# Performance work log

Measured on AMD Instinct MI355X. Metric: run time of the kernel, lower is better.

The kernel has to match this reference:

```python
import jax, jax.numpy as jnp
import numpy as np

B, T, D = 2, 4096, 768
H = 12
DK = D // H


def setup_inputs() -> dict:
    key = jax.random.key(0)
    k1, k2, k3 = jax.random.split(key, 3)
    x = jax.random.normal(k1, (B, T, D), dtype=jnp.float32)
    W_qkv = jax.random.normal(k2, (D, 3 * D), dtype=jnp.float32) * (1.0 / np.sqrt(D))
    b_qkv = jnp.zeros((3 * D,), dtype=jnp.float32)
    W_proj = jax.random.normal(k3, (D, D), dtype=jnp.float32) * (1.0 / np.sqrt(D))
    b_proj = jnp.zeros((D,), dtype=jnp.float32)
    return {"x": x, "W_qkv": W_qkv, "b_qkv": b_qkv, "W_proj": W_proj, "b_proj": b_proj}


def reference(x, W_qkv, b_qkv, W_proj, b_proj):
    b, t, c = x.shape
    qkv = x @ W_qkv + b_qkv                      # [B,T,3D]
    q, k, v = jnp.split(qkv, 3, axis=-1)
    q = q.reshape(b, t, H, DK)                   # [B,T,H,DK]
    k = k.reshape(b, t, H, DK)
    v = v.reshape(b, t, H, DK)
    scale = 1.0 / np.sqrt(DK)
    scores = jnp.einsum('bthd,bshd->bhts', q, k) * scale   # [B,H,T,T]
    causal = jnp.tril(jnp.ones((t, t), dtype=bool))
    scores = jnp.where(causal[None, None], scores, jnp.float32(-jnp.inf))
    probs = jax.nn.softmax(scores, axis=-1)      # dropout p=0.0 -> identity
    out = jnp.einsum('bhts,bshd->bthd', probs, v).reshape(b, t, c)
    return out @ W_proj + b_proj
```

## Files before the change

kernel.cpp:

```cpp
#include <hip/hip_runtime.h>
#include <hip/hip_bf16.h>
#include <cstdint>
#include <cstddef>


typedef __attribute__((ext_vector_type(8))) short bf16x8;
typedef __attribute__((ext_vector_type(4))) short bf16x4;
typedef __attribute__((ext_vector_type(4))) float f32x4;

#define MFMA16(a, b, c)   __builtin_amdgcn_mfma_f32_16x16x32_bf16((a), (b), (c), 0, 0, 0)
#define MFMA16K(a, b, c)  __builtin_amdgcn_mfma_f32_16x16x16bf16_1k((a), (b), (c), 0, 0, 0)

static constexpr int Bc = 2, Tc = 4096, Dc = 768, Hc = 12, DKc = 64;
static constexpr int BHc = Bc * Hc;
static constexpr int Mc = Bc * Tc;
static constexpr int Nqkv = 3 * Dc;
static constexpr int NQBLK = Tc / 128;
static constexpr unsigned int NITEMS = BHc * NQBLK;

__device__ __forceinline__ unsigned short f2bf(float f) {
    union { float f; unsigned int i; } c; c.f = f;
    unsigned int x = c.i;
    return (unsigned short)((x + 0x7fffu + ((x >> 16) & 1u)) >> 16);
}
__device__ __forceinline__ unsigned int pkbf(float a, float b) {
    __hip_bfloat162 h = __float22bfloat162_rn(make_float2(a, b));
    union { __hip_bfloat162 h; unsigned int u; } c; c.h = h;
    return c.u;
}
__device__ __forceinline__ void glds16(const unsigned short* g, unsigned short* l) {
    __builtin_amdgcn_global_load_lds(
        (const __attribute__((address_space(1))) unsigned int*)g,
        (__attribute__((address_space(3))) unsigned int*)l, 16, 0, 0);
}

__global__ __launch_bounds__(256)
void xconv_kernel(const float* __restrict__ X, unsigned short* __restrict__ Xb) {
    size_t i = ((size_t)blockIdx.x * 256 + threadIdx.x) * 8;
    float4 a = *(const float4*)(X + i);
    float4 b = *(const float4*)(X + i + 4);
    uint4 o;
    o.x = pkbf(a.x, a.y); o.y = pkbf(a.z, a.w);
    o.z = pkbf(b.x, b.y); o.w = pkbf(b.z, b.w);
    *(uint4*)(Xb + i) = o;
}

__global__ __launch_bounds__(256)
void wtrans_kernel(const float* __restrict__ Wq, const float* __restrict__ Wp,
                   unsigned short* __restrict__ WqT, unsigned short* __restrict__ WpT) {
    __shared__ __align__(16) unsigned short tile[64 * 72];
    const int k0 = blockIdx.x * 64;
    const int yb = blockIdx.y;
    const float* W;
    unsigned short* WT;
    int N, n0;
    if (yb < 36) { W = Wq; WT = WqT; N = Nqkv; n0 = yb * 64; }
    else         { W = Wp; WT = WpT; N = Dc;   n0 = (yb - 36) * 64; }
    const int tid = threadIdx.x;
#pragma unroll
    for (int it = 0; it < 4; ++it) {
        int s = tid + it * 256;
        int r = s >> 4, g = s & 15;
        float4 v = *(const float4*)(W + (size_t)(k0 + r) * N + n0 + g * 4);
        ushort4 u;
        u.x = f2bf(v.x); u.y = f2bf(v.y); u.z = f2bf(v.z); u.w = f2bf(v.w);
        *(ushort4*)(tile + r * 72 + g * 4) = u;
    }
    __syncthreads();
#pragma unroll
    for (int it = 0; it < 2; ++it) {
        int s = tid + it * 256;
        int n = s >> 3, g = s & 7;
        unsigned int p0 = (unsigned int)tile[(g * 8 + 0) * 72 + n] |
                          ((unsigned int)tile[(g * 8 + 1) * 72 + n] << 16);
        unsigned int p1 = (unsigned int)tile[(g * 8 + 2) * 72 + n] |
                          ((unsigned int)tile[(g * 8 + 3) * 72 + n] << 16);
        unsigned int p2 = (unsigned int)tile[(g * 8 + 4) * 72 + n] |
                          ((unsigned int)tile[(g * 8 + 5) * 72 + n] << 16);
        unsigned int p3 = (unsigned int)tile[(g * 8 + 6) * 72 + n] |
                          ((unsigned int)tile[(g * 8 + 7) * 72 + n] << 16);
        uint4 o; o.x = p0; o.y = p1; o.z = p2; o.w = p3;
        *(uint4*)(WT + (size_t)(n0 + n) * Dc + k0 + g * 8) = o;
    }
}

__global__ __launch_bounds__(256)
void qkv_gemm_kernel(const unsigned short* __restrict__ Xb,
                     const unsigned short* __restrict__ WT,
                     const float* __restrict__ bias,
                     unsigned short* __restrict__ Qb, unsigned short* __restrict__ Kb,
                     unsigned short* __restrict__ Vt) {
    __shared__ __align__(16) unsigned short As[128 * 64];
    __shared__ __align__(16) unsigned short Bs[128 * 64];
    const int tid = threadIdx.x;
    const int wave = tid >> 6, lane = tid & 63;
    const int quad = lane >> 4, l15 = lane & 15;
    const int wr = wave >> 1, wc = wave & 1;
    const int r0 = blockIdx.x * 128, c0 = blockIdx.y * 128;
    const int sw = l15 & 7;

    f32x4 acc[4][4];
#pragma unroll
    for (int i = 0; i < 4; ++i)
#pragma unroll
        for (int j = 0; j < 4; ++j) acc[i][j] = (f32x4){0.f, 0.f, 0.f, 0.f};

    for (int k0 = 0; k0 < Dc; k0 += 64) {
#pragma unroll
        for (int it = 0; it < 4; ++it) {
            int idx = it * 256 + tid;
            int r = idx >> 3, c = idx & 7;
            int cg = c ^ (r & 7);
            glds16(Xb + (size_t)(r0 + r) * Dc + k0 + cg * 8, As + idx * 8);
            glds16(WT + (size_t)(c0 + r) * Dc + k0 + cg * 8, Bs + idx * 8);
        }
        __syncthreads();
#pragma unroll
        for (int f = 0; f < 2; ++f) {
            bf16x8 af[4], bfr[4];
#pragma unroll
            for (int mt = 0; mt < 4; ++mt)
                af[mt] = *(const bf16x8*)(As + (wr * 64 + mt * 16 + l15) * 64 +
                                          (((f * 4 + quad) ^ sw) * 8));
#pragma unroll
            for (int nt = 0; nt < 4; ++nt)
                bfr[nt] = *(const bf16x8*)(Bs + (wc * 64 + nt * 16 + l15) * 64 +
                                           (((f * 4 + quad) ^ sw) * 8));
#pragma unroll
            for (int mt = 0; mt < 4; ++mt)
#pragma unroll
                for (int nt = 0; nt < 4; ++nt)
                    acc[mt][nt] = MFMA16(af[mt], bfr[nt], acc[mt][nt]);
        }
        __syncthreads();
    }

    const int part = c0 / Dc;
    const int cbase = c0 - part * Dc;
    const float scale = (part == 0) ? 0.125f * 1.4426950408889634f : 1.0f;
    float bv[4];
#pragma unroll
    for (int nt = 0; nt < 4; ++nt) bv[nt] = bias[c0 + wc * 64 + nt * 16 + l15];

    if (part < 2) {
        unsigned short* dstbuf = (part == 0) ? Qb : Kb;
#pragma unroll
        for (int mt = 0; mt < 4; ++mt)
#pragma unroll
            for (int reg = 0; reg < 4; ++reg) {
                int gr = r0 + wr * 64 + mt * 16 + quad * 4 + reg;
                int b = gr >> 12, t = gr & 4095;
#pragma unroll
                for (int nt = 0; nt < 4; ++nt) {
                    int cc = cbase + wc * 64 + nt * 16 + l15;
                    int h = cc >> 6, dk = cc & 63;
                    float v = (acc[mt][nt][reg] + bv[nt]) * scale;
                    dstbuf[((size_t)(b * Hc + h) * Tc + t) * DKc + dk] = f2bf(v);
                }
            }
    } else {
#pragma unroll
        for (int mt = 0; mt < 4; ++mt)
#pragma unroll
            for (int reg = 0; reg < 4; ++reg) {
                int gr = r0 + wr * 64 + mt * 16 + quad * 4 + reg;
                int b = gr >> 12, t = gr & 4095;
#pragma unroll
                for (int nt = 0; nt < 4; ++nt) {
                    int cc = cbase + wc * 64 + nt * 16 + l15;
                    int h = cc >> 6, dk = cc & 63;
                    float v = acc[mt][nt][reg] + bv[nt];
                    Vt[((size_t)(b * Hc + h) * DKc + dk) * Tc + t] = f2bf(v);
                }
            }
    }
}

__global__ __launch_bounds__(256)
void attn_kernel(const unsigned short* __restrict__ Qb,
                 const unsigned short* __restrict__ Kb,
                 const unsigned short* __restrict__ Vt,
                 unsigned short* __restrict__ attn,
                 unsigned int* __restrict__ counter) {
    __shared__ __align__(16) unsigned short Ks[64 * 64];
    __shared__ __align__(16) unsigned short Vs[64 * 64];
    __shared__ unsigned int s_w;
    const int tid = threadIdx.x;
    const int wave = tid >> 6, lane = tid & 63;
    const int quad = lane >> 4, l15 = lane & 15;
    const int sw = l15 & 7;
    const f32x4 czero = (f32x4){0.f, 0.f, 0.f, 0.f};
    const bf16x4 ones = (bf16x4){(short)0x3F80, (short)0x3F80,
                                 (short)0x3F80, (short)0x3F80};

    for (;;) {
        if (tid == 0) s_w = atomicAdd(counter, 1u);
        __syncthreads();
        const unsigned int w = s_w;
        if (w >= NITEMS) break;
        const int bh = (int)(w % (unsigned)BHc);
        const int i0 = (NQBLK - 1 - (int)(w / (unsigned)BHc)) * 128;
        const unsigned short* Qp = Qb + (size_t)bh * Tc * DKc;
        const unsigned short* Kp = Kb + (size_t)bh * Tc * DKc;
        const unsigned short* Vp = Vt + (size_t)bh * DKc * Tc;

        bf16x8 qf[2][2];
#pragma unroll
        for (int qg = 0; qg < 2; ++qg)
#pragma unroll
            for (int f = 0; f < 2; ++f)
                qf[qg][f] = *(const bf16x8*)(Qp +
                    (size_t)(i0 + wave * 32 + qg * 16 + l15) * DKc + f * 32 + quad * 8);

        f32x4 lsum[2] = {czero, czero};
        f32x4 o[2][4];
#pragma unroll
        for (int qg = 0; qg < 2; ++qg)
#pragma unroll
            for (int d = 0; d < 4; ++d) o[qg][d] = (f32x4){0.f, 0.f, 0.f, 0.f};

        const int jmax = (i0 >> 6) + 1;
        for (int jt = 0; jt <= jmax; ++jt) {
            const int j0 = jt * 64;
#pragma unroll
            for (int it = 0; it < 2; ++it) {
                int idx = it * 256 + tid;
                int r = idx >> 3, c = idx & 7;
                int cg = c ^ (r & 7);
                glds16(Kp + (size_t)(j0 + r) * DKc + cg * 8, Ks + idx * 8);
                glds16(Vp + (size_t)r * Tc + j0 + cg * 8, Vs + idx * 8);
            }
            __syncthreads();

            bf16x8 kf[2][4];
            bf16x4 vf[4][4];
#pragma unroll
            for (int f = 0; f < 2; ++f)
#pragma unroll
                for (int mt = 0; mt < 4; ++mt)
                    kf[f][mt] = *(const bf16x8*)(Ks + (mt * 16 + l15) * 64 +
                                                 (((f * 4 + quad) ^ sw) * 8));
#pragma unroll
            for (int d = 0; d < 4; ++d)
#pragma unroll
                for (int mt = 0; mt < 4; ++mt) {
                    int g8 = mt * 4 + quad;
                    vf[d][mt] = *(const bf16x4*)(Vs + (d * 16 + l15) * 64 +
                                                 (((g8 >> 1) ^ sw) * 8) + (g8 & 1) * 4);
                }
            asm volatile("s_waitcnt lgkmcnt(0)" ::: "memory");
            __builtin_amdgcn_s_barrier();

            f32x4 sc[2][4];
#pragma unroll
            for (int mt = 0; mt < 4; ++mt) {
                sc[0][mt] = MFMA16(kf[0][mt], qf[0][0], czero);
                sc[1][mt] = MFMA16(kf[0][mt], qf[1][0], czero);
            }
#pragma unroll
            for (int mt = 0; mt < 4; ++mt) {
                sc[0][mt] = MFMA16(kf[1][mt], qf[0][1], sc[0][mt]);
                sc[1][mt] = MFMA16(kf[1][mt], qf[1][1], sc[1][mt]);
            }

            const int rel = j0 - i0;
            if (jt >= jmax - 1) {
#pragma unroll
                for (int qg = 0; qg < 2; ++qg) {
                    int qrow = wave * 32 + qg * 16 + l15;
#pragma unroll
                    for (int mt = 0; mt < 4; ++mt)
#pragma unroll
                        for (int reg = 0; reg < 4; ++reg)
                            if (rel + mt * 16 + quad * 4 + reg > qrow)
                                sc[qg][mt][reg] = -1e30f;
                }
            }

            union { uint2 u; bf16x4 v; } pb[2][4];
#pragma unroll
            for (int qg = 0; qg < 2; ++qg)
#pragma unroll
                for (int mt = 0; mt < 4; ++mt) {
#pragma unroll
                    for (int reg = 0; reg < 4; ++reg)
                        sc[qg][mt][reg] = __builtin_amdgcn_exp2f(sc[qg][mt][reg]);
                    pb[qg][mt].u.x = pkbf(sc[qg][mt][0], sc[qg][mt][1]);
                    pb[qg][mt].u.y = pkbf(sc[qg][mt][2], sc[qg][mt][3]);
                }

#pragma unroll
            for (int mt = 0; mt < 4; ++mt) {
                lsum[0] = MFMA16K(ones, pb[0][mt].v, lsum[0]);
                lsum[1] = MFMA16K(ones, pb[1][mt].v, lsum[1]);
#pragma unroll
                for (int d = 0; d < 4; ++d) {
                    o[0][d] = MFMA16K(vf[d][mt], pb[0][mt].v, o[0][d]);
                    o[1][d] = MFMA16K(vf[d][mt], pb[1][mt].v, o[1][d]);
                }
            }
        }

        const int b = bh / Hc, h = bh % Hc;
#pragma unroll
        for (int qg = 0; qg < 2; ++qg) {
            float li = 1.0f / lsum[qg][0];
            int t = i0 + wave * 32 + qg * 16 + l15;
            unsigned short* dst = attn + (size_t)(b * Tc + t) * Dc + h * 64;
#pragma unroll
            for (int d = 0; d < 4; ++d) {
                uint2 u;
                u.x = pkbf(o[qg][d][0] * li, o[qg][d][1] * li);
                u.y = pkbf(o[qg][d][2] * li, o[qg][d][3] * li);
                *(uint2*)(dst + d * 16 + quad * 4) = u;
            }
        }
    }
}

__global__ __launch_bounds__(256)
void proj_gemm_kernel(const unsigned short* __restrict__ A,
                      const unsigned short* __restrict__ WT,
                      const float* __restrict__ bias, float* __restrict__ out) {
    __shared__ __align__(16) unsigned short As[128 * 64];
    __shared__ __align__(16) unsigned short Bs[64 * 64];
    const int tid = threadIdx.x;
    const int wave = tid >> 6, lane = tid & 63;
    const int quad = lane >> 4, l15 = lane & 15;
    const int wr = wave >> 1, wc = wave & 1;
    const int r0 = blockIdx.x * 128, c0 = blockIdx.y * 64;
    const int sw = l15 & 7;

    f32x4 acc[4][2];
#pragma unroll
    for (int i = 0; i < 4; ++i)
#pragma unroll
        for (int j = 0; j < 2; ++j) acc[i][j] = (f32x4){0.f, 0.f, 0.f, 0.f};

    for (int k0 = 0; k0 < Dc; k0 += 64) {
#pragma unroll
        for (int it = 0; it < 4; ++it) {
            int idx = it * 256 + tid;
            int r = idx >> 3, c = idx & 7;
            glds16(A + (size_t)(r0 + r) * Dc + k0 + ((c ^ (r & 7)) * 8), As + idx * 8);
        }
#pragma unroll
        for (int it = 0; it < 2; ++it) {
            int idx = it * 256 + tid;
            int r = idx >> 3, c = idx & 7;
            glds16(WT + (size_t)(c0 + r) * Dc + k0 + ((c ^ (r & 7)) * 8), Bs + idx * 8);
        }
        __syncthreads();
#pragma unroll
        for (int f = 0; f < 2; ++f) {
            bf16x8 af[4], bfr[2];
#pragma unroll
            for (int mt = 0; mt < 4; ++mt)
                af[mt] = *(const bf16x8*)(As + (wr * 64 + mt * 16 + l15) * 64 +
                                          (((f * 4 + quad) ^ sw) * 8));
#pragma unroll
            for (int nt = 0; nt < 2; ++nt)
                bfr[nt] = *(const bf16x8*)(Bs + (wc * 32 + nt * 16 + l15) * 64 +
                                           (((f * 4 + quad) ^ sw) * 8));
#pragma unroll
            for (int mt = 0; mt < 4; ++mt)
#pragma unroll
                for (int nt = 0; nt < 2; ++nt)
                    acc[mt][nt] = MFMA16(af[mt], bfr[nt], acc[mt][nt]);
        }
        __syncthreads();
    }

    float bv[2];
#pragma unroll
    for (int nt = 0; nt < 2; ++nt) bv[nt] = bias[c0 + wc * 32 + nt * 16 + l15];
#pragma unroll
    for (int mt = 0; mt < 4; ++mt)
#pragma unroll
        for (int reg = 0; reg < 4; ++reg) {
            int gr = r0 + wr * 64 + mt * 16 + quad * 4 + reg;
#pragma unroll
            for (int nt = 0; nt < 2; ++nt) {
                int gc = c0 + wc * 32 + nt * 16 + l15;
                out[(size_t)gr * Dc + gc] = acc[mt][nt][reg] + bv[nt];
            }
        }
}

extern "C" void kernel_launch(void* const* d_in, const int* in_sizes, int n_in,
                              void* d_out, int out_size, void* d_ws, size_t ws_size,
                              hipStream_t stream) {
    const float* x      = (const float*)d_in[0];
    const float* W_qkv  = (const float*)d_in[1];
    const float* b_qkv  = (const float*)d_in[2];
    const float* W_proj = (const float*)d_in[3];
    const float* b_proj = (const float*)d_in[4];
    float* out = (float*)d_out;

    char* ws = (char*)d_ws;
    size_t off = 0;
    auto take = [&](size_t bytes) -> char* {
        char* p = ws + off;
        off += (bytes + 255) & ~(size_t)255;
        return p;
    };
    unsigned int*   cnt = (unsigned int*)take(256);
    unsigned short* WqT = (unsigned short*)take((size_t)Nqkv * Dc * 2);
    unsigned short* WpT = (unsigned short*)take((size_t)Dc * Dc * 2);
    unsigned short* Qb  = (unsigned short*)take((size_t)BHc * Tc * DKc * 2);
    unsigned short* Kb  = (unsigned short*)take((size_t)BHc * Tc * DKc * 2);
    unsigned short* Vt  = (unsigned short*)take((size_t)BHc * Tc * DKc * 2);
    unsigned short* Xb  = (unsigned short*)take((size_t)Mc * Dc * 2);
    unsigned short* An  = Xb;

    hipMemsetAsync(cnt, 0, sizeof(unsigned int), stream);
    xconv_kernel<<<dim3((Mc * Dc) / (256 * 8)), dim3(256), 0, stream>>>(x, Xb);
    wtrans_kernel<<<dim3(Dc / 64, (Nqkv + Dc) / 64), dim3(256), 0, stream>>>(W_qkv, W_proj, WqT, WpT);
    qkv_gemm_kernel<<<dim3(Mc / 128, Nqkv / 128), dim3(256), 0, stream>>>(Xb, WqT, b_qkv, Qb, Kb, Vt);
    attn_kernel<<<dim3(NITEMS), dim3(256), 0, stream>>>(Qb, Kb, Vt, An, cnt);
    proj_gemm_kernel<<<dim3(Mc / 128, Dc / 64), dim3(256), 0, stream>>>(An, WpT, b_proj, out);
}
```

Measured before the change: 253.6 us.

## Split causal attention key range into two halves with flag-based partial merge

Each 128-row query block except the first is split into two work items that each cover half of the key tiles. Each half writes its unnormalized output and row sums to a float workspace. An atomic per-pair flag picks whichever half finishes second to merge both partials, normalize, and write the bf16 output. The aim is to shorten the longest work items and balance the causal triangle across CUs. In exchange it adds extra global writes and reads for the partials, fences, and a 4-blocks-per-CU launch bound that may force register spills.

```diff
diff --git a/kernel.cpp b/kernel.cpp
--- a/kernel.cpp
+++ b/kernel.cpp
@@ -16,7 +16,9 @@
 static constexpr int Mc = Bc * Tc;
 static constexpr int Nqkv = 3 * Dc;
 static constexpr int NQBLK = Tc / 128;
-static constexpr unsigned int NITEMS = BHc * NQBLK;
+static constexpr unsigned int NSPLIT = 24u * 31u * 2u;
+static constexpr unsigned int NIT = NSPLIT + 24u;
+static constexpr int NPAIR = 31 * 24;
 
 __device__ __forceinline__ unsigned short f2bf(float f) {
     union { float f; unsigned int i; } c; c.f = f;
@@ -176,15 +178,18 @@
     }
 }
 
-__global__ __launch_bounds__(256)
+__global__ __launch_bounds__(256, 4)
 void attn_kernel(const unsigned short* __restrict__ Qb,
                  const unsigned short* __restrict__ Kb,
                  const unsigned short* __restrict__ Vt,
                  unsigned short* __restrict__ attn,
-                 unsigned int* __restrict__ counter) {
+                 unsigned int* __restrict__ counter,
+                 unsigned int* __restrict__ flags,
+                 float* __restrict__ Opart,
+                 float* __restrict__ Lpart) {
     __shared__ __align__(16) unsigned short Ks[64 * 64];
     __shared__ __align__(16) unsigned short Vs[64 * 64];
-    __shared__ unsigned int s_w;
+    __shared__ unsigned int s_w, s_role;
     const int tid = threadIdx.x;
     const int wave = tid >> 6, lane = tid & 63;
     const int quad = lane >> 4, l15 = lane & 15;
@@ -197,9 +202,21 @@
         if (tid == 0) s_w = atomicAdd(counter, 1u);
         __syncthreads();
         const unsigned int w = s_w;
-        if (w >= NITEMS) break;
-        const int bh = (int)(w % (unsigned)BHc);
-        const int i0 = (NQBLK - 1 - (int)(w / (unsigned)BHc)) * 128;
+        if (w >= NIT) break;
+        int qb, bh, half;
+        bool split;
+        if (w < NSPLIT) {
+            int g = (int)(w / 48u);
+            int r = (int)(w - (unsigned)g * 48u);
+            qb = 31 - g; bh = r >> 1; half = r & 1; split = true;
+        } else {
+            bh = (int)(w - NSPLIT); qb = 0; half = 0; split = false;
+        }
+        const int T = qb + 1;
+        const int i0 = qb * 128;
+        const int jbeg = split ? half * T : 0;
+        const int jend = split ? jbeg + T : 2;
+
         const unsigned short* Qp = Qb + (size_t)bh * Tc * DKc;
         const unsigned short* Kp = Kb + (size_t)bh * Tc * DKc;
         const unsigned short* Vp = Vt + (size_t)bh * DKc * Tc;
@@ -219,8 +236,7 @@
 #pragma unroll
             for (int d = 0; d < 4; ++d) o[qg][d] = (f32x4){0.f, 0.f, 0.f, 0.f};
 
-        const int jmax = (i0 >> 6) + 1;
-        for (int jt = 0; jt <= jmax; ++jt) {
+        for (int jt = jbeg; jt < jend; ++jt) {
             const int j0 = jt * 64;
 #pragma unroll
             for (int it = 0; it < 2; ++it) {
@@ -263,8 +279,8 @@
                 sc[1][mt] = MFMA16(kf[1][mt], qf[1][1], sc[1][mt]);
             }
 
-            const int rel = j0 - i0;
-            if (jt >= jmax - 1) {
+            if (jt >= 2 * T - 2) {
+                const int rel = j0 - i0;
 #pragma unroll
                 for (int qg = 0; qg < 2; ++qg) {
                     int qrow = wave * 32 + qg * 16 + l15;
@@ -302,17 +318,69 @@
         }
 
         const int b = bh / Hc, h = bh % Hc;
-#pragma unroll
-        for (int qg = 0; qg < 2; ++qg) {
-            float li = 1.0f / lsum[qg][0];
-            int t = i0 + wave * 32 + qg * 16 + l15;
-            unsigned short* dst = attn + (size_t)(b * Tc + t) * Dc + h * 64;
-#pragma unroll
-            for (int d = 0; d < 4; ++d) {
-                uint2 u;
-                u.x = pkbf(o[qg][d][0] * li, o[qg][d][1] * li);
-                u.y = pkbf(o[qg][d][2] * li, o[qg][d][3] * li);
-                *(uint2*)(dst + d * 16 + quad * 4) = u;
+        if (!split) {
+#pragma unroll
+            for (int qg = 0; qg < 2; ++qg) {
+                float li = 1.0f / lsum[qg][0];
+                int t = i0 + wave * 32 + qg * 16 + l15;
+                unsigned short* dst = attn + (size_t)(b * Tc + t) * Dc + h * 64;
+#pragma unroll
+                for (int d = 0; d < 4; ++d) {
+                    uint2 u;
+                    u.x = pkbf(o[qg][d][0] * li, o[qg][d][1] * li);
+                    u.y = pkbf(o[qg][d][2] * li, o[qg][d][3] * li);
+                    *(uint2*)(dst + d * 16 + quad * 4) = u;
+                }
+            }
+        } else {
+            const int pid = (qb - 1) * 24 + bh;
+            float* Ob = Opart + ((size_t)pid * 2 + half) * (64 * 128);
+            float* Lb = Lpart + ((size_t)pid * 2 + half) * 128;
+#pragma unroll
+            for (int qg = 0; qg < 2; ++qg) {
+                int row = wave * 32 + qg * 16 + l15;
+#pragma unroll
+                for (int d = 0; d < 4; ++d)
+#pragma unroll
+                    for (int reg = 0; reg < 4; ++reg)
+                        __hip_atomic_store(&Ob[(d * 16 + quad * 4 + reg) * 128 + row],
+                                           o[qg][d][reg], __ATOMIC_RELAXED,
+                                           __HIP_MEMORY_SCOPE_AGENT);
+                if (quad == 0)
+                    __hip_atomic_store(&Lb[row], lsum[qg][0], __ATOMIC_RELAXED,
+                                       __HIP_MEMORY_SCOPE_AGENT);
+            }
+            __threadfence();
+            __syncthreads();
+            if (tid == 0) s_role = atomicAdd(&flags[pid], 1u);
+            __syncthreads();
+            if (s_role == 1u) {
+                __threadfence();
+                const float* Po = Opart + ((size_t)pid * 2 + (half ^ 1)) * (64 * 128);
+                const float* Pl = Lpart + ((size_t)pid * 2 + (half ^ 1)) * 128;
+#pragma unroll
+                for (int qg = 0; qg < 2; ++qg) {
+                    int row = wave * 32 + qg * 16 + l15;
+                    float pl = __hip_atomic_load(&Pl[row], __ATOMIC_RELAXED,
+                                                 __HIP_MEMORY_SCOPE_AGENT);
+#pragma unroll
+                    for (int d = 0; d < 4; ++d)
+#pragma unroll
+                        for (int reg = 0; reg < 4; ++reg)
+                            o[qg][d][reg] += __hip_atomic_load(
+                                &Po[(d * 16 + quad * 4 + reg) * 128 + row],
+                                __ATOMIC_RELAXED, __HIP_MEMORY_SCOPE_AGENT);
+                    float li = 1.0f / (lsum[qg][0] + pl);
+                    int t = i0 + row;
+                    unsigned short* dst = attn + (size_t)(b * Tc + t) * Dc + h * 64;
+#pragma unroll
+                    for (int d = 0; d < 4; ++d) {
+                        uint2 u;
+                        u.x = pkbf(o[qg][d][0] * li, o[qg][d][1] * li);
+                        u.y = pkbf(o[qg][d][2] * li, o[qg][d][3] * li);
+                        *(uint2*)(dst + d * 16 + quad * 4) = u;
+                    }
+                }
             }
         }
     }
@@ -404,19 +472,22 @@
         off += (bytes + 255) & ~(size_t)255;
         return p;
     };
-    unsigned int*   cnt = (unsigned int*)take(256);
+    unsigned int*   cnt = (unsigned int*)take(4096);
+    unsigned int*   flg = cnt + 64;
     unsigned short* WqT = (unsigned short*)take((size_t)Nqkv * Dc * 2);
     unsigned short* WpT = (unsigned short*)take((size_t)Dc * Dc * 2);
     unsigned short* Qb  = (unsigned short*)take((size_t)BHc * Tc * DKc * 2);
     unsigned short* Kb  = (unsigned short*)take((size_t)BHc * Tc * DKc * 2);
     unsigned short* Vt  = (unsigned short*)take((size_t)BHc * Tc * DKc * 2);
     unsigned short* Xb  = (unsigned short*)take((size_t)Mc * Dc * 2);
+    float*          Op  = (float*)take((size_t)NPAIR * 2 * 64 * 128 * 4);
+    float*          Lp  = (float*)take((size_t)NPAIR * 2 * 128 * 4);
     unsigned short* An  = Xb;
 
-    hipMemsetAsync(cnt, 0, sizeof(unsigned int), stream);
+    hipMemsetAsync(cnt, 0, 4096, stream);
     xconv_kernel<<<dim3((Mc * Dc) / (256 * 8)), dim3(256), 0, stream>>>(x, Xb);
     wtrans_kernel<<<dim3(Dc / 64, (Nqkv + Dc) / 64), dim3(256), 0, stream>>>(W_qkv, W_proj, WqT, WpT);
     qkv_gemm_kernel<<<dim3(Mc / 128, Nqkv / 128), dim3(256), 0, stream>>>(Xb, WqT, b_qkv, Qb, Kb, Vt);
-    attn_kernel<<<dim3(NITEMS), dim3(256), 0, stream>>>(Qb, Kb, Vt, An, cnt);
+    attn_kernel<<<dim3(NIT), dim3(256), 0, stream>>>(Qb, Kb, Vt, An, cnt, flg, Op, Lp);
     proj_gemm_kernel<<<dim3(Mc / 128, Dc / 64), dim3(256), 0, stream>>>(An, WpT, b_proj, out);
 }
```

New measurement: 757.4 us. 199% more time.
